# Kernel optimization log

Hardware: AMD Instinct MI355X
Metric: run time of the kernel (lower is better)

## Reference

```python
import jax, jax.numpy as jnp
import numpy as np

B = 256
N = 1024
K = 64
BASIS = 8
SINKHORN_ITERS = 1
TEMP = 0.2
EPS = 1e-5


def log_sinkhorn(log_alpha, n_iters=SINKHORN_ITERS, temperature=TEMP):
    la = log_alpha / temperature
    for _ in range(n_iters):
        la = la - jax.scipy.special.logsumexp(la, axis=-1, keepdims=True)
        la = la - jax.scipy.special.logsumexp(la, axis=-2, keepdims=True)
    return jnp.exp(la)


def setup_inputs() -> dict:
    key = jax.random.key(0)
    k1, k2, k3, k4 = jax.random.split(key, 4)
    x = jax.random.normal(k1, (B, N * K), dtype=jnp.float32)
    A_logits = 0.01 * jax.random.normal(k2, (N, N), dtype=jnp.float32)
    W_1 = 0.01 * jax.random.normal(k3, (N, BASIS), dtype=jnp.float32)
    W_V = 0.01 * jax.random.normal(k4, (BASIS, K, K), dtype=jnp.float32)
    gamma2 = jnp.ones((N,), dtype=jnp.float32)  # LayerNorm(N) weight
    beta2 = jnp.zeros((N,), dtype=jnp.float32)  # LayerNorm(N) bias
    return {"x": x, "A_logits": A_logits, "W_1": W_1, "W_V": W_V,
            "gamma2": gamma2, "beta2": beta2}


def layernorm(x, gamma, beta):
    mu = jnp.mean(x, axis=-1, keepdims=True)
    var = jnp.mean(jnp.square(x - mu), axis=-1, keepdims=True)
    return (x - mu) * jax.lax.rsqrt(var + EPS) * gamma + beta


def reference(x, A_logits, W_1, W_V, gamma2, beta2):
    x_reshaped = x.reshape(B, N, K)
    A = log_sinkhorn(A_logits)                       # [N, N] doubly-stochastic
    W_logits = jnp.einsum('tk,kde->tde', W_1, W_V)   # [N, K, K]
    W = log_sinkhorn(W_logits)                       # per-block doubly-stochastic
    x_local = jnp.einsum('bni,nio->bno', x_reshaped, W)  # N independent KxK GEMMs
    x_local = layernorm(jnp.transpose(x_local, (0, 2, 1)), gamma2, beta2)  # [B,K,N]
    x_global = x_local @ A                           # [B,K,N]
    x_global = jnp.transpose(x_global, (0, 2, 1))    # [B,N,K]
    return x_global.reshape(B, N * K)
```

## Files before the change

kernel.cpp:

```cpp
#include <hip/hip_runtime.h>
#include <hip/hip_fp16.h>
#include <math.h>

#define NDIM 1024
#define KDIM 64
#define BDIM 256
#define BKDIM 16384

typedef unsigned short u16;
typedef __attribute__((ext_vector_type(8))) short bf16x8;
typedef __attribute__((ext_vector_type(4))) float f32x4;

__device__ __forceinline__ float bf2f(u16 u) {
  union { unsigned u; float f; } x; x.u = ((unsigned)u) << 16; return x.f;
}
__device__ __forceinline__ u16 f2bf(float f) {
  union { float f; unsigned u; } x; x.f = f;
  unsigned u = x.u;
  u += 0x7fffu + ((u >> 16) & 1u);
  return (u16)(u >> 16);
}

__device__ __forceinline__ void async16(const u16* g, u16* s) {
  __builtin_amdgcn_global_load_lds(
      (const __attribute__((address_space(1))) unsigned int*)g,
      (__attribute__((address_space(3))) unsigned int*)s,
      16, 0, 0);
}

__global__ __launch_bounds__(256) void k_pre(const float* __restrict__ Alog,
                                             float* __restrict__ r,
                                             const float* __restrict__ W1,
                                             const float* __restrict__ WV,
                                             u16* __restrict__ Wt) {
  __shared__ float sred[256];
  __shared__ float sla[64 * 65];
  int t = threadIdx.x;
  if (blockIdx.x < 1024) {
    int m = blockIdx.x;
    float v[4], mx = -3.0e38f;
#pragma unroll
    for (int j = 0; j < 4; j++) {
      v[j] = Alog[m * NDIM + t + j * 256] * 5.0f;
      mx = fmaxf(mx, v[j]);
    }
    sred[t] = mx; __syncthreads();
    for (int s = 128; s > 0; s >>= 1) { if (t < s) sred[t] = fmaxf(sred[t], sred[t + s]); __syncthreads(); }
    float bm = sred[0]; __syncthreads();
    float sm = 0.f;
#pragma unroll
    for (int j = 0; j < 4; j++) sm += __expf(v[j] - bm);
    sred[t] = sm; __syncthreads();
    for (int s = 128; s > 0; s >>= 1) { if (t < s) sred[t] += sred[t + s]; __syncthreads(); }
    if (t == 0) r[m] = bm + __logf(sred[0]);
  } else {
    int tb = blockIdx.x - 1024;
    int d = t >> 2, q = t & 3;
    float w1[8];
#pragma unroll
    for (int k = 0; k < 8; k++) w1[k] = W1[tb * 8 + k];
    float la[16];
#pragma unroll
    for (int j = 0; j < 16; j++) la[j] = 0.f;
#pragma unroll
    for (int k = 0; k < 8; k++) {
      float wk = w1[k];
      const float4* base = (const float4*)&WV[k * 4096 + d * 64 + q * 16];
#pragma unroll
      for (int v = 0; v < 4; v++) {
        float4 f = base[v];
        la[v * 4 + 0] += wk * f.x; la[v * 4 + 1] += wk * f.y;
        la[v * 4 + 2] += wk * f.z; la[v * 4 + 3] += wk * f.w;
      }
    }
    float mx = -3.0e38f;
#pragma unroll
    for (int j = 0; j < 16; j++) { la[j] *= 5.0f; mx = fmaxf(mx, la[j]); }
    float sm = 0.f;
#pragma unroll
    for (int j = 0; j < 16; j++) sm += __expf(la[j] - mx);
    for (int off = 1; off < 4; off <<= 1) {
      float mo = __shfl_xor(mx, off), so = __shfl_xor(sm, off);
      float mn = fmaxf(mx, mo);
      sm = sm * __expf(mx - mn) + so * __expf(mo - mn);
      mx = mn;
    }
    float rl = mx + __logf(sm);
#pragma unroll
    for (int j = 0; j < 16; j++) sla[d * 65 + q * 16 + j] = la[j] - rl;
    __syncthreads();
    int e = t >> 2, jj = t & 3;
    float lb[16]; float m2 = -3.0e38f;
#pragma unroll
    for (int i = 0; i < 16; i++) { lb[i] = sla[(jj * 16 + i) * 65 + e]; m2 = fmaxf(m2, lb[i]); }
    float s2 = 0.f;
#pragma unroll
    for (int i = 0; i < 16; i++) s2 += __expf(lb[i] - m2);
    for (int off = 1; off < 4; off <<= 1) {
      float mo = __shfl_xor(m2, off), so = __shfl_xor(s2, off);
      float mn = fmaxf(m2, mo);
      s2 = s2 * __expf(m2 - mn) + so * __expf(mo - mn);
      m2 = mn;
    }
    float cl = m2 + __logf(s2);
#pragma unroll
    for (int i = 0; i < 16; i++)
      Wt[tb * 4096 + e * 64 + jj * 16 + i] = f2bf(__expf(lb[i] - cl));
  }
}

__global__ __launch_bounds__(256, 2) void k_gemm1c(const float* __restrict__ x,
                                                   const u16* __restrict__ Wt,
                                                   u16* __restrict__ xln) {
  int bx = blockIdx.x, bt = blockIdx.y, t = threadIdx.x;
  int n8 = (bx & 15) * 8 + (bx >> 4);
  int w = t >> 6, l = t & 63, q = l >> 4, lr = l & 15;
  int n0 = n8 * 8;
  const float* xb = x + (size_t)(bt * 64 + w * 16 + lr) * 65536 + n0 * 64;
  f32x4 acc[8][4] = {};
#pragma unroll
  for (int n = 0; n < 8; n++) {
#pragma unroll
    for (int ks = 0; ks < 2; ks++) {
      const float* xr = xb + n * 64 + ks * 32 + q * 8;
      float4 v0 = *(const float4*)xr;
      float4 v1 = *(const float4*)(xr + 4);
      float vf[8] = {v0.x, v0.y, v0.z, v0.w, v1.x, v1.y, v1.z, v1.w};
      bf16x8 ah, al;
#pragma unroll
      for (int j = 0; j < 8; j++) {
        u16 h = f2bf(vf[j]);
        ah[j] = (short)h;
        al[j] = (short)f2bf(vf[j] - bf2f(h));
      }
#pragma unroll
      for (int ni = 0; ni < 4; ni++) {
        bf16x8 bfr = *(const bf16x8*)&Wt[(size_t)(n0 + n) * 4096 + (ni * 16 + lr) * 64 + ks * 32 + q * 8];
        acc[n][ni] = __builtin_amdgcn_mfma_f32_16x16x32_bf16(ah, bfr, acc[n][ni], 0, 0, 0);
        acc[n][ni] = __builtin_amdgcn_mfma_f32_16x16x32_bf16(al, bfr, acc[n][ni], 0, 0, 0);
      }
    }
  }
#pragma unroll
  for (int ni = 0; ni < 4; ni++) {
#pragma unroll
    for (int reg = 0; reg < 4; reg++) {
      int bk = (bt * 64 + w * 16 + q * 4 + reg) * 64 + ni * 16 + lr;
      bf16x8 o;
#pragma unroll
      for (int n = 0; n < 8; n++) o[n] = (short)f2bf(acc[n][ni][reg]);
      *(bf16x8*)&xln[(size_t)bk * 1024 + n0] = o;
    }
  }
}

__global__ __launch_bounds__(256) void k_col_dt2(const float* __restrict__ Alog,
                                                 const float* __restrict__ r,
                                                 const float* __restrict__ g2,
                                                 const float* __restrict__ b2,
                                                 u16* __restrict__ Dt,
                                                 float* __restrict__ gAc,
                                                 float* __restrict__ bAc) {
  int n = blockIdx.x, t = threadIdx.x;
  float v[4], mx = -3.0e38f;
#pragma unroll
  for (int j = 0; j < 4; j++) {
    int m = t + j * 256;
    v[j] = Alog[m * NDIM + n] * 5.0f - r[m];
    mx = fmaxf(mx, v[j]);
  }
  __shared__ float sred[256];
  sred[t] = mx; __syncthreads();
  for (int s = 128; s > 0; s >>= 1) { if (t < s) sred[t] = fmaxf(sred[t], sred[t + s]); __syncthreads(); }
  float bm = sred[0]; __syncthreads();
  float sm = 0.f;
#pragma unroll
  for (int j = 0; j < 4; j++) sm += __expf(v[j] - bm);
  sred[t] = sm; __syncthreads();
  for (int s = 128; s > 0; s >>= 1) { if (t < s) sred[t] += sred[t + s]; __syncthreads(); }
  float cn = bm + __logf(sred[0]);
  float ga = 0.f, ba = 0.f;
#pragma unroll
  for (int j = 0; j < 4; j++) {
    int m = t + j * 256;
    float e = __expf(v[j] - cn);
    float gm = g2[m];
    Dt[n * NDIM + m] = f2bf(gm * (e - 0.0009765625f));
    ga += gm * e; ba += b2[m] * e;
  }
  __syncthreads();
  sred[t] = ga; __syncthreads();
  for (int s = 128; s > 0; s >>= 1) { if (t < s) sred[t] += sred[t + s]; __syncthreads(); }
  if (t == 0) gAc[n] = sred[0];
  __syncthreads();
  sred[t] = ba; __syncthreads();
  for (int s = 128; s > 0; s >>= 1) { if (t < s) sred[t] += sred[t + s]; __syncthreads(); }
  if (t == 0) bAc[n] = sred[0];
}

__global__ __launch_bounds__(256) void k_stat3(const u16* __restrict__ xln,
                                               const float* __restrict__ g2,
                                               float* __restrict__ e1,
                                               float* __restrict__ e2,
                                               float* __restrict__ e3) {
  int t = threadIdx.x;
  int row = blockIdx.x * 16 + (t >> 4);
  int c = t & 15;
  const u16* xr = xln + (size_t)row * 1024 + c * 8;
  float S = 0.f, Q = 0.f, W = 0.f;
#pragma unroll
  for (int j = 0; j < 8; j++) {
    bf16x8 v = *(const bf16x8*)&xr[j * 128];
    const float* gp = g2 + j * 128 + c * 8;
    float4 g0 = *(const float4*)gp;
    float4 g1 = *(const float4*)(gp + 4);
    float gg[8] = {g0.x, g0.y, g0.z, g0.w, g1.x, g1.y, g1.z, g1.w};
#pragma unroll
    for (int k = 0; k < 8; k++) {
      float f = bf2f((u16)v[k]);
      S += f; Q += f * f; W += f * gg[k];
    }
  }
#pragma unroll
  for (int off = 1; off < 16; off <<= 1) {
    S += __shfl_xor(S, off);
    Q += __shfl_xor(Q, off);
    W += __shfl_xor(W, off);
  }
  if (c == 0) {
    float m_ = S * (1.0f / 1024.0f);
    float var = Q * (1.0f / 1024.0f) - m_ * m_;
    float a = rsqrtf(var + 1e-5f);
    e1[row] = a;
    e2[row] = a * W * (1.0f / 1024.0f);
    e3[row] = -a * m_;
  }
}

__global__ __launch_bounds__(256) void k_gemm2g(const u16* __restrict__ Dt,
                                                const u16* __restrict__ xln,
                                                const float* __restrict__ e1,
                                                const float* __restrict__ e2,
                                                const float* __restrict__ e3,
                                                const float* __restrict__ gAc,
                                                const float* __restrict__ bAc,
                                                float* __restrict__ out) {
  __shared__ __align__(16) u16 lA[128 * 64];
  __shared__ __align__(16) u16 lB[128 * 64];
  int bkt = blockIdx.x, n2t = blockIdx.y;
  int t = threadIdx.x, w = t >> 6, l = t & 63;
  int q = l >> 4, lr = l & 15;
  int rr = l >> 3;
  int cc = (l & 7) ^ rr;
  const u16* gAp = Dt  + (size_t)(n2t * 128) * NDIM + cc * 8;
  const u16* gBp = xln + (size_t)(bkt * 128) * NDIM + cc * 8;
  f32x4 acc[4][4] = {};
  for (int kt = 0; kt < 16; kt++) {
#pragma unroll
    for (int j = 0; j < 4; j++) {
      int ci = j * 4 + w;
      int row = ci * 8 + rr;
      async16(gAp + (size_t)row * NDIM + kt * 64, &lA[ci * 512 + l * 8]);
      async16(gBp + (size_t)row * NDIM + kt * 64, &lB[ci * 512 + l * 8]);
    }
    __syncthreads();
#pragma unroll
    for (int ks = 0; ks < 2; ks++) {
      int pc = ((ks * 4 + q) ^ (lr & 7)) * 8;
      bf16x8 af[4], bfr[4];
#pragma unroll
      for (int mi = 0; mi < 4; mi++)
        af[mi] = *(const bf16x8*)&lA[((w >> 1) * 64 + mi * 16 + lr) * 64 + pc];
#pragma unroll
      for (int ni = 0; ni < 4; ni++)
        bfr[ni] = *(const bf16x8*)&lB[((w & 1) * 64 + ni * 16 + lr) * 64 + pc];
#pragma unroll
      for (int mi = 0; mi < 4; mi++)
#pragma unroll
        for (int ni = 0; ni < 4; ni++)
          acc[mi][ni] = __builtin_amdgcn_mfma_f32_16x16x32_bf16(af[mi], bfr[ni], acc[mi][ni], 0, 0, 0);
    }
    __syncthreads();
  }
  float* sE = (float*)lA;
  if (t < 128) {
    sE[t]       = e1[bkt * 128 + t];
    sE[128 + t] = e2[bkt * 128 + t];
    sE[256 + t] = e3[bkt * 128 + t];
    sE[384 + t] = gAc[n2t * 128 + t];
    sE[512 + t] = bAc[n2t * 128 + t];
  }
  __syncthreads();
  float a1v[4], a2v[4], a3v[4];
#pragma unroll
  for (int ni = 0; ni < 4; ni++) {
    int bkl = (w & 1) * 64 + ni * 16 + lr;
    a1v[ni] = sE[bkl]; a2v[ni] = sE[128 + bkl]; a3v[ni] = sE[256 + bkl];
  }
  int bkb = bkt * 128 + (w & 1) * 64 + lr;
#pragma unroll
  for (int mi = 0; mi < 4; mi++) {
    __builtin_amdgcn_sched_barrier(0);
#pragma unroll
    for (int reg = 0; reg < 4; reg++) {
      int n2l = (w >> 1) * 64 + mi * 16 + q * 4 + reg;
      float gg = sE[384 + n2l], bb = sE[512 + n2l];
      int n2 = n2t * 128 + n2l;
#pragma unroll
      for (int ni = 0; ni < 4; ni++) {
        int bk = bkb + ni * 16;
        int b = bk >> 6, o = bk & 63;
        out[(size_t)b * 65536 + n2 * 64 + o] =
            a1v[ni] * acc[mi][ni][reg] + a2v[ni] + a3v[ni] * gg + bb;
      }
    }
  }
}

extern "C" void kernel_launch(void* const* d_in, const int* in_sizes, int n_in,
                              void* d_out, int out_size, void* d_ws, size_t ws_size,
                              hipStream_t stream) {
  const float* x    = (const float*)d_in[0];
  const float* Alog = (const float*)d_in[1];
  const float* W1   = (const float*)d_in[2];
  const float* WV   = (const float*)d_in[3];
  const float* g2   = (const float*)d_in[4];
  const float* b2   = (const float*)d_in[5];
  float* out = (float*)d_out;
  char* ws = (char*)d_ws;

  u16*   xln = (u16*)(ws);
  u16*   Wt  = (u16*)(ws + 33554432ull);
  float* e1  = (float*)(ws + 33554432ull);
  float* e2  = (float*)(ws + 33619968ull);
  float* e3  = (float*)(ws + 33685504ull);
  u16*   Dt  = (u16*)(ws + 41943040ull);
  float* r   = (float*)(ws + 44040192ull);
  float* gAc = (float*)(ws + 44044288ull);
  float* bAc = (float*)(ws + 44048384ull);

  k_pre<<<dim3(2048), dim3(256), 0, stream>>>(Alog, r, W1, WV, Wt);
  k_gemm1c<<<dim3(128, 4), dim3(256), 0, stream>>>(x, Wt, xln);
  k_col_dt2<<<dim3(1024), dim3(256), 0, stream>>>(Alog, r, g2, b2, Dt, gAc, bAc);
  k_stat3<<<dim3(1024), dim3(256), 0, stream>>>(xln, g2, e1, e2, e3);
  k_gemm2g<<<dim3(128, 8), dim3(256), 0, stream>>>(Dt, xln, e1, e2, e3, gAc, bAc, out);
}
```

Measured before the change: 224.5 us.

## Split gemm1 across 512-thread blocks and fuse column-softmax with row stats kernel

```diff
diff --git a/kernel.cpp b/kernel.cpp
--- a/kernel.cpp
+++ b/kernel.cpp
@@ -9,6 +9,7 @@
 
 typedef unsigned short u16;
 typedef __attribute__((ext_vector_type(8))) short bf16x8;
+typedef __attribute__((ext_vector_type(4))) short bf16x4;
 typedef __attribute__((ext_vector_type(4))) float f32x4;
 
 __device__ __forceinline__ float bf2f(u16 u) {
@@ -109,17 +110,19 @@
   }
 }
 
-__global__ __launch_bounds__(256, 2) void k_gemm1c(const float* __restrict__ x,
+__global__ __launch_bounds__(512, 4) void k_gemm1d(const float* __restrict__ x,
                                                    const u16* __restrict__ Wt,
                                                    u16* __restrict__ xln) {
   int bx = blockIdx.x, bt = blockIdx.y, t = threadIdx.x;
   int n8 = (bx & 15) * 8 + (bx >> 4);
   int w = t >> 6, l = t & 63, q = l >> 4, lr = l & 15;
-  int n0 = n8 * 8;
-  const float* xb = x + (size_t)(bt * 64 + w * 16 + lr) * 65536 + n0 * 64;
-  f32x4 acc[8][4] = {};
-#pragma unroll
-  for (int n = 0; n < 8; n++) {
+  int p = w & 3, h = w >> 2;
+  int nb = n8 * 8 + h * 4;
+  const float* xb = x + (size_t)(bt * 64 + p * 16 + lr) * 65536;
+  f32x4 acc[4][4] = {};
+#pragma unroll
+  for (int np = 0; np < 4; np++) {
+    int n = nb + np;
 #pragma unroll
     for (int ks = 0; ks < 2; ks++) {
       const float* xr = xb + n * 64 + ks * 32 + q * 8;
@@ -129,15 +132,15 @@
       bf16x8 ah, al;
 #pragma unroll
       for (int j = 0; j < 8; j++) {
-        u16 h = f2bf(vf[j]);
-        ah[j] = (short)h;
-        al[j] = (short)f2bf(vf[j] - bf2f(h));
+        u16 hh = f2bf(vf[j]);
+        ah[j] = (short)hh;
+        al[j] = (short)f2bf(vf[j] - bf2f(hh));
       }
 #pragma unroll
       for (int ni = 0; ni < 4; ni++) {
-        bf16x8 bfr = *(const bf16x8*)&Wt[(size_t)(n0 + n) * 4096 + (ni * 16 + lr) * 64 + ks * 32 + q * 8];
-        acc[n][ni] = __builtin_amdgcn_mfma_f32_16x16x32_bf16(ah, bfr, acc[n][ni], 0, 0, 0);
-        acc[n][ni] = __builtin_amdgcn_mfma_f32_16x16x32_bf16(al, bfr, acc[n][ni], 0, 0, 0);
+        bf16x8 bfr = *(const bf16x8*)&Wt[(size_t)n * 4096 + (ni * 16 + lr) * 64 + ks * 32 + q * 8];
+        acc[np][ni] = __builtin_amdgcn_mfma_f32_16x16x32_bf16(ah, bfr, acc[np][ni], 0, 0, 0);
+        acc[np][ni] = __builtin_amdgcn_mfma_f32_16x16x32_bf16(al, bfr, acc[np][ni], 0, 0, 0);
       }
     }
   }
@@ -145,95 +148,95 @@
   for (int ni = 0; ni < 4; ni++) {
 #pragma unroll
     for (int reg = 0; reg < 4; reg++) {
-      int bk = (bt * 64 + w * 16 + q * 4 + reg) * 64 + ni * 16 + lr;
-      bf16x8 o;
-#pragma unroll
-      for (int n = 0; n < 8; n++) o[n] = (short)f2bf(acc[n][ni][reg]);
-      *(bf16x8*)&xln[(size_t)bk * 1024 + n0] = o;
-    }
-  }
-}
-
-__global__ __launch_bounds__(256) void k_col_dt2(const float* __restrict__ Alog,
-                                                 const float* __restrict__ r,
-                                                 const float* __restrict__ g2,
-                                                 const float* __restrict__ b2,
-                                                 u16* __restrict__ Dt,
-                                                 float* __restrict__ gAc,
-                                                 float* __restrict__ bAc) {
-  int n = blockIdx.x, t = threadIdx.x;
-  float v[4], mx = -3.0e38f;
-#pragma unroll
-  for (int j = 0; j < 4; j++) {
-    int m = t + j * 256;
-    v[j] = Alog[m * NDIM + n] * 5.0f - r[m];
-    mx = fmaxf(mx, v[j]);
-  }
+      int bk = (bt * 64 + p * 16 + q * 4 + reg) * 64 + ni * 16 + lr;
+      bf16x4 o;
+#pragma unroll
+      for (int np = 0; np < 4; np++) o[np] = (short)f2bf(acc[np][ni][reg]);
+      *(bf16x4*)&xln[(size_t)bk * 1024 + nb] = o;
+    }
+  }
+}
+
+__global__ __launch_bounds__(256) void k_post(const float* __restrict__ Alog,
+                                              const float* __restrict__ r,
+                                              const float* __restrict__ g2,
+                                              const float* __restrict__ b2,
+                                              u16* __restrict__ Dt,
+                                              float* __restrict__ gAc,
+                                              float* __restrict__ bAc,
+                                              const u16* __restrict__ xln,
+                                              float* __restrict__ e1,
+                                              float* __restrict__ e2,
+                                              float* __restrict__ e3) {
   __shared__ float sred[256];
-  sred[t] = mx; __syncthreads();
-  for (int s = 128; s > 0; s >>= 1) { if (t < s) sred[t] = fmaxf(sred[t], sred[t + s]); __syncthreads(); }
-  float bm = sred[0]; __syncthreads();
-  float sm = 0.f;
-#pragma unroll
-  for (int j = 0; j < 4; j++) sm += __expf(v[j] - bm);
-  sred[t] = sm; __syncthreads();
-  for (int s = 128; s > 0; s >>= 1) { if (t < s) sred[t] += sred[t + s]; __syncthreads(); }
-  float cn = bm + __logf(sred[0]);
-  float ga = 0.f, ba = 0.f;
-#pragma unroll
-  for (int j = 0; j < 4; j++) {
-    int m = t + j * 256;
-    float e = __expf(v[j] - cn);
-    float gm = g2[m];
-    Dt[n * NDIM + m] = f2bf(gm * (e - 0.0009765625f));
-    ga += gm * e; ba += b2[m] * e;
-  }
-  __syncthreads();
-  sred[t] = ga; __syncthreads();
-  for (int s = 128; s > 0; s >>= 1) { if (t < s) sred[t] += sred[t + s]; __syncthreads(); }
-  if (t == 0) gAc[n] = sred[0];
-  __syncthreads();
-  sred[t] = ba; __syncthreads();
-  for (int s = 128; s > 0; s >>= 1) { if (t < s) sred[t] += sred[t + s]; __syncthreads(); }
-  if (t == 0) bAc[n] = sred[0];
-}
-
-__global__ __launch_bounds__(256) void k_stat3(const u16* __restrict__ xln,
-                                               const float* __restrict__ g2,
-                                               float* __restrict__ e1,
-                                               float* __restrict__ e2,
-                                               float* __restrict__ e3) {
   int t = threadIdx.x;
-  int row = blockIdx.x * 16 + (t >> 4);
-  int c = t & 15;
-  const u16* xr = xln + (size_t)row * 1024 + c * 8;
-  float S = 0.f, Q = 0.f, W = 0.f;
-#pragma unroll
-  for (int j = 0; j < 8; j++) {
-    bf16x8 v = *(const bf16x8*)&xr[j * 128];
-    const float* gp = g2 + j * 128 + c * 8;
-    float4 g0 = *(const float4*)gp;
-    float4 g1 = *(const float4*)(gp + 4);
-    float gg[8] = {g0.x, g0.y, g0.z, g0.w, g1.x, g1.y, g1.z, g1.w};
-#pragma unroll
-    for (int k = 0; k < 8; k++) {
-      float f = bf2f((u16)v[k]);
-      S += f; Q += f * f; W += f * gg[k];
-    }
-  }
-#pragma unroll
-  for (int off = 1; off < 16; off <<= 1) {
-    S += __shfl_xor(S, off);
-    Q += __shfl_xor(Q, off);
-    W += __shfl_xor(W, off);
-  }
-  if (c == 0) {
-    float m_ = S * (1.0f / 1024.0f);
-    float var = Q * (1.0f / 1024.0f) - m_ * m_;
-    float a = rsqrtf(var + 1e-5f);
-    e1[row] = a;
-    e2[row] = a * W * (1.0f / 1024.0f);
-    e3[row] = -a * m_;
+  if (blockIdx.x < 1024) {
+    int n = blockIdx.x;
+    float v[4], mx = -3.0e38f;
+#pragma unroll
+    for (int j = 0; j < 4; j++) {
+      int m = t + j * 256;
+      v[j] = Alog[m * NDIM + n] * 5.0f - r[m];
+      mx = fmaxf(mx, v[j]);
+    }
+    sred[t] = mx; __syncthreads();
+    for (int s = 128; s > 0; s >>= 1) { if (t < s) sred[t] = fmaxf(sred[t], sred[t + s]); __syncthreads(); }
+    float bm = sred[0]; __syncthreads();
+    float sm = 0.f;
+#pragma unroll
+    for (int j = 0; j < 4; j++) sm += __expf(v[j] - bm);
+    sred[t] = sm; __syncthreads();
+    for (int s = 128; s > 0; s >>= 1) { if (t < s) sred[t] += sred[t + s]; __syncthreads(); }
+    float cn = bm + __logf(sred[0]);
+    float ga = 0.f, ba = 0.f;
+#pragma unroll
+    for (int j = 0; j < 4; j++) {
+      int m = t + j * 256;
+      float e = __expf(v[j] - cn);
+      float gm = g2[m];
+      Dt[n * NDIM + m] = f2bf(gm * (e - 0.0009765625f));
+      ga += gm * e; ba += b2[m] * e;
+    }
+    __syncthreads();
+    sred[t] = ga; __syncthreads();
+    for (int s = 128; s > 0; s >>= 1) { if (t < s) sred[t] += sred[t + s]; __syncthreads(); }
+    if (t == 0) gAc[n] = sred[0];
+    __syncthreads();
+    sred[t] = ba; __syncthreads();
+    for (int s = 128; s > 0; s >>= 1) { if (t < s) sred[t] += sred[t + s]; __syncthreads(); }
+    if (t == 0) bAc[n] = sred[0];
+  } else {
+    int row = (blockIdx.x - 1024) * 16 + (t >> 4);
+    int c = t & 15;
+    const u16* xr = xln + (size_t)row * 1024 + c * 8;
+    float S = 0.f, Q = 0.f, W = 0.f;
+#pragma unroll
+    for (int j = 0; j < 8; j++) {
+      bf16x8 v = *(const bf16x8*)&xr[j * 128];
+      const float* gp = g2 + j * 128 + c * 8;
+      float4 g0 = *(const float4*)gp;
+      float4 g1 = *(const float4*)(gp + 4);
+      float gg[8] = {g0.x, g0.y, g0.z, g0.w, g1.x, g1.y, g1.z, g1.w};
+#pragma unroll
+      for (int k = 0; k < 8; k++) {
+        float f = bf2f((u16)v[k]);
+        S += f; Q += f * f; W += f * gg[k];
+      }
+    }
+#pragma unroll
+    for (int off = 1; off < 16; off <<= 1) {
+      S += __shfl_xor(S, off);
+      Q += __shfl_xor(Q, off);
+      W += __shfl_xor(W, off);
+    }
+    if (c == 0) {
+      float m_ = S * (1.0f / 1024.0f);
+      float var = Q * (1.0f / 1024.0f) - m_ * m_;
+      float a = rsqrtf(var + 1e-5f);
+      e1[row] = a;
+      e2[row] = a * W * (1.0f / 1024.0f);
+      e3[row] = -a * m_;
+    }
   }
 }
 
@@ -340,8 +343,7 @@
   float* bAc = (float*)(ws + 44048384ull);
 
   k_pre<<<dim3(2048), dim3(256), 0, stream>>>(Alog, r, W1, WV, Wt);
-  k_gemm1c<<<dim3(128, 4), dim3(256), 0, stream>>>(x, Wt, xln);
-  k_col_dt2<<<dim3(1024), dim3(256), 0, stream>>>(Alog, r, g2, b2, Dt, gAc, bAc);
-  k_stat3<<<dim3(1024), dim3(256), 0, stream>>>(xln, g2, e1, e2, e3);
+  k_gemm1d<<<dim3(128, 4), dim3(512), 0, stream>>>(x, Wt, xln);
+  k_post<<<dim3(2048), dim3(256), 0, stream>>>(Alog, r, g2, b2, Dt, gAc, bAc, xln, e1, e2, e3);
   k_gemm2g<<<dim3(128, 8), dim3(256), 0, stream>>>(Dt, xln, e1, e2, e3, gAc, bAc, out);
 }
```

Measured after the change: 224.2 us. Within noise of the previous version (-0.2%).
